# Optimization experiments

Hardware: AMD Instinct MI355X
Metric: run time of the kernel (lower is better)

Reference implementation:

```python
import jax, jax.numpy as jnp
import numpy as np

NUM_HEADS = 8
CHUNK = 64          # dialtion / chunck_size
EPS = 1e-5          # InstanceNorm1d eps
NEG = -1e9


def setup_inputs() -> dict:
    key = jax.random.key(0)
    ks = jax.random.split(key, 8)
    N, C, T = 4, 512, 4096
    x = jax.random.normal(ks[0], (N, C, T), dtype=jnp.float32)
    q = jax.random.normal(ks[1], (N, C, T), dtype=jnp.float32)
    k = jax.random.normal(ks[2], (N, C, T), dtype=jnp.float32)
    v = jax.random.normal(ks[3], (N, C, T), dtype=jnp.float32)
    masks = jnp.ones((N, 1, T), dtype=jnp.float32)
    s = 1.0 / np.sqrt(C)
    W_in = jax.random.normal(ks[4], (3 * C, C), dtype=jnp.float32) * s   # packed q/k/v in-proj
    b_in = jnp.zeros((3 * C,), dtype=jnp.float32)
    W_out = jax.random.normal(ks[5], (C, C), dtype=jnp.float32) * s     # out-proj
    b_out = jnp.zeros((C,), dtype=jnp.float32)
    return {"x": x, "q": q, "k": k, "v": v, "masks": masks,
            "W_in": W_in, "b_in": b_in, "W_out": W_out, "b_out": b_out}


def _chunk_attn(q, k, v, masks, W_in, b_in, W_out, b_out):
    # q,k,v: [N, C, T]; masks: [N, 1, T]
    N, C, T = q.shape
    H, Dh = NUM_HEADS, C // NUM_HEADS
    nc = T // CHUNK
    Wq, Wk, Wv = jnp.split(W_in, 3, axis=0)
    bq, bk, bv = jnp.split(b_in, 3, axis=0)

    def proj(t, W, b):
        # [N,C,T] -> chunked heads [N, nc, CHUNK, H, Dh]
        t = t.transpose(0, 2, 1) @ W.T + b            # [N, T, C]
        return t.reshape(N, nc, CHUNK, H, Dh)

    qh = proj(q, Wq, bq)
    kh = proj(k, Wk, bk)
    vh = proj(v, Wv, bv)

    scale = 1.0 / jnp.sqrt(jnp.asarray(Dh, q.dtype))
    # intra-chunk scores: [N, nc, H, CHUNK, CHUNK]
    scores = jnp.einsum('bnqhd,bnkhd->bnhqk', qh, kh) * scale
    km = masks[:, 0, :].reshape(N, nc, CHUNK)         # key validity per chunk
    scores = scores + jnp.where(km[:, :, None, None, :] > 0, 0.0, NEG)
    attn = jax.nn.softmax(scores, axis=-1)
    out = jnp.einsum('bnhqk,bnkhd->bnqhd', attn, vh).reshape(N, T, C)
    out = out @ W_out.T + b_out                        # [N, T, C]
    out = out.transpose(0, 2, 1) * masks               # [N, C, T], re-mask
    return out


def reference(x, q, k, v, masks, W_in, b_in, W_out, b_out):
    out = _chunk_attn(q, k, v, masks, W_in, b_in, W_out, b_out) + x
    # InstanceNorm1d (affine=False): normalize each (n, c) row over T
    mu = jnp.mean(out, axis=2, keepdims=True)
    var = jnp.mean(jnp.square(out - mu), axis=2, keepdims=True)
    return (out - mu) * jax.lax.rsqrt(var + EPS)
```

## Files before the change

### kernel.cpp

```cpp
#include <hip/hip_runtime.h>
#include <hip/hip_bf16.h>

#define NB 4
#define CC 512
#define TT 4096
#define C3 1536
#define CQK 1024
#define NTC (NB*TT*CC)

typedef __attribute__((ext_vector_type(4))) float f32x4;
typedef __attribute__((ext_vector_type(8))) short short8;
typedef unsigned short ushort;
typedef __attribute__((ext_vector_type(8))) ushort u16x8;

__device__ __forceinline__ ushort f2bf(float f){
    union { float f; unsigned u; } x; x.f = f;
    unsigned r = x.u + 0x7fffu + ((x.u >> 16) & 1u);
    return (ushort)(r >> 16);
}

__device__ __forceinline__ ushort2 pk2bf(float a, float b){
    float2 f2; f2.x = a; f2.y = b;
    __hip_bfloat162 h = __float22bfloat162_rn(f2);
    union { __hip_bfloat162 h2; ushort2 u2; } u; u.h2 = h;
    return u.u2;
}

__device__ __forceinline__ void gload16(const void* g, void* l){
    __builtin_amdgcn_global_load_lds((const __attribute__((address_space(1))) void*)g,
                                     (__attribute__((address_space(3))) void*)l,
                                     16, 0, 0);
}

__device__ __forceinline__ int apos(int m, int cb){
    return (m*8 + ((cb + m + (m >> 3)) & 7))*8;
}

__global__ __launch_bounds__(256) void wcvt(const float* __restrict__ Wi,
                                            const float* __restrict__ Wo,
                                            ushort* __restrict__ Wb,
                                            ushort* __restrict__ Wob){
    int idx0 = blockIdx.x * 1024 + threadIdx.x;
    for (int i = 0; i < 4; ++i){
        int idx = idx0 + i*256;
        const float* src; ushort* dst; int j;
        if (idx < 196608){ src = Wi; dst = Wb;  j = idx; }
        else             { src = Wo; dst = Wob; j = idx - 196608; }
        f32x4 vv = *((const f32x4*)src + j);
        ushort4 o;
        *(ushort2*)&o.x = pk2bf(vv[0], vv[1]);
        *(ushort2*)&o.z = pk2bf(vv[2], vv[3]);
        *((ushort4*)dst + j) = o;
    }
}

__global__ __launch_bounds__(256) void proj_gemm(const float* __restrict__ q,
                                                 const float* __restrict__ k,
                                                 const float* __restrict__ v,
                                                 const ushort* __restrict__ Wb,
                                                 const float* __restrict__ b_in,
                                                 ushort* __restrict__ P,
                                                 ushort* __restrict__ Vt){
    __shared__ __align__(16) ushort smem[40960];
    ushort* sA   = smem;
    ushort* sB0  = smem + 8192;
    ushort* sB1  = smem + 16384;
    float*  Araw = (float*)(smem + 24576);
    const int tid = threadIdx.x;
    const int bid = blockIdx.x;
    const int mtile  = ((bid & 7) << 4) | ((bid >> 3) & 15);
    const int cotile = bid >> 7;
    const int co0 = cotile * 128;
    const int m0  = mtile * 128;
    const int which = co0 >> 9;
    const float* src = (which == 0) ? q : (which == 1) ? k : v;
    const int n  = m0 >> 12, t0 = m0 & 4095;
    const ushort* Bbase = Wb + (size_t)co0*CC;
    const int w = tid >> 6, lane = tid & 63;
    const int wr = w >> 1, wc = w & 1;
    const int l15 = lane & 15, quad = lane >> 4;

    const int rowoff = lane >> 5;
    const int toff   = (lane & 31) * 4;
    const float* Ag = src + (size_t)n*CC*TT + (size_t)(2*w + rowoff)*TT + t0 + toff;
    float* lAr = Araw + (size_t)(2*w)*128;

    const ushort* gB[4]; int lBoff[4];
    for (int i = 0; i < 4; ++i){
        int slot = i*256 + tid;
        int mr = slot >> 3, k8 = slot & 7, kk = k8 ^ (mr & 7);
        gB[i] = Bbase + (size_t)mr*CC + kk*8;
        lBoff[i] = (i*256 + (tid & ~63)) * 8;
    }

    const int cbA = (w << 1) | (lane >> 5);
    const int tA  = lane & 31;

    for (int r = 0; r < 8; ++r)
        gload16(Ag + (size_t)(r*8)*TT, lAr + r*1024);
    for (int i = 0; i < 4; ++i)
        gload16(gB[i], sB0 + lBoff[i]);

    f32x4 acc[4][4] = {};
    for (int kb = 0; kb < 8; ++kb){
        ushort* sBc = (kb & 1) ? sB1 : sB0;
        ushort* sBn = (kb & 1) ? sB0 : sB1;
        __syncthreads();
        f32x4 cur[8];
        #pragma unroll
        for (int j = 0; j < 8; ++j)
            cur[j] = *(const f32x4*)(Araw + (size_t)(cbA*8 + j)*128 + tA*4);
        #pragma unroll
        for (int tj = 0; tj < 4; ++tj){
            int m = tA*4 + tj;
            u16x8 o;
            #pragma unroll
            for (int j = 0; j < 8; j += 2){
                ushort2 p = pk2bf(cur[j][tj], cur[j+1][tj]);
                o[j] = p.x; o[j+1] = p.y;
            }
            *(u16x8*)&sA[apos(m, cbA)] = o;
        }
        __syncthreads();
        if (kb < 7){
            const float* Agn = Ag + (size_t)((kb+1)*64)*TT;
            for (int r = 0; r < 8; ++r)
                gload16(Agn + (size_t)(r*8)*TT, lAr + r*1024);
            for (int i = 0; i < 4; ++i)
                gload16(gB[i] + (kb+1)*64, sBn + lBoff[i]);
        }
        for (int ks = 0; ks < 2; ++ks){
            short8 aF[4], bF[4];
            for (int mi = 0; mi < 4; ++mi){
                int m = wr*64 + mi*16 + l15;
                aF[mi] = *(const short8*)&sA[apos(m, ks*4 + quad)];
            }
            for (int ni = 0; ni < 4; ++ni){
                int m = wc*64 + ni*16 + l15;
                bF[ni] = *(const short8*)&sBc[(m*8 + ((ks*4 + quad) ^ (m & 7)))*8];
            }
            for (int mi = 0; mi < 4; ++mi)
                for (int ni = 0; ni < 4; ++ni)
                    acc[mi][ni] = __builtin_amdgcn_mfma_f32_16x16x32_bf16(
                        aF[mi], bF[ni], acc[mi][ni], 0, 0, 0);
        }
    }

    float bj[4];
    for (int ni = 0; ni < 4; ++ni) bj[ni] = b_in[co0 + wc*64 + ni*16 + l15];

    __syncthreads();
    ushort* sOut = smem;
    if (which < 2){
        for (int mi = 0; mi < 4; ++mi){
            int mrow = wr*64 + mi*16 + quad*4;
            for (int ni = 0; ni < 4; ++ni){
                int col = wc*64 + ni*16 + l15;
                for (int r = 0; r < 4; ++r)
                    sOut[(mrow + r)*136 + col] = f2bf(acc[mi][ni][r] + bj[ni]);
            }
        }
    } else {
        for (int mi = 0; mi < 4; ++mi){
            int mrow = wr*64 + mi*16 + quad*4;
            for (int ni = 0; ni < 4; ++ni){
                int col = wc*64 + ni*16 + l15;
                ushort4 o4;
                o4.x = f2bf(acc[mi][ni][0] + bj[ni]);
                o4.y = f2bf(acc[mi][ni][1] + bj[ni]);
                o4.z = f2bf(acc[mi][ni][2] + bj[ni]);
                o4.w = f2bf(acc[mi][ni][3] + bj[ni]);
                *(ushort4*)&sOut[col*136 + mrow] = o4;
            }
        }
    }
    __syncthreads();
    if (which < 2){
        for (int i = 0; i < 8; ++i){
            int flat = i*256 + tid;
            int row = flat >> 4, cs = (flat & 15)*8;
            u16x8 val = *(const u16x8*)&sOut[row*136 + cs];
            *(u16x8*)(P + (size_t)(m0 + row)*CQK + which*512 + (co0 & 511) + cs) = val;
        }
    } else {
        for (int i = 0; i < 8; ++i){
            int flat = i*256 + tid;
            int row = flat >> 4, cs = (flat & 15)*8;
            int cl = (co0 - 1024) + row;
            int h = cl >> 6, d = cl & 63;
            u16x8 val = *(const u16x8*)&sOut[row*136 + cs];
            *(u16x8*)(Vt + (((size_t)n*8 + h)*64 + d)*TT + t0 + cs) = val;
        }
    }
}

__global__ __launch_bounds__(256) void attn_kernel(const ushort* __restrict__ P,
                                                   const ushort* __restrict__ Vt,
                                                   const float* __restrict__ masks,
                                                   ushort* __restrict__ ctx){
    __shared__ __align__(16) ushort sQ[64*64], sK[64*64], sV[64*64];
    __shared__ __align__(16) ushort sP[64][72];
    __shared__ __align__(16) ushort sO[64*72];
    int bid = blockIdx.x;
    int h = bid & 7, ch = (bid >> 3) & 63, n = bid >> 9;
    const int tid = threadIdx.x, lane = tid & 63, w = tid >> 6;
    const int l15 = lane & 15, quad = lane >> 4;
    const size_t rowbase = (size_t)n*TT + (size_t)ch*64;
    for (int i = 0; i < 2; ++i){
        int slot = i*256 + tid;
        int r = slot >> 3, k8 = slot & 7, kk = k8 ^ (r & 7);
        int lbase = (i*256 + (tid & ~63)) * 8;
        const ushort* gq = P + (rowbase + r)*CQK + h*64 + kk*8;
        gload16(gq,        sQ + lbase);
        gload16(gq + 512,  sK + lbase);
        const ushort* gv = Vt + (((size_t)n*8 + h)*64 + r)*TT + ch*64 + kk*8;
        gload16(gv,        sV + lbase);
    }
    __syncthreads();
    const int m0w = w*16;
    short8 aQ[2]; f32x4 accS[4] = {};
    for (int ks = 0; ks < 2; ++ks){
        int m = m0w + l15;
        aQ[ks] = *(const short8*)&sQ[(m*8 + ((ks*4 + quad) ^ (m & 7)))*8];
    }
    for (int ni = 0; ni < 4; ++ni)
        for (int ks = 0; ks < 2; ++ks){
            int m = ni*16 + l15;
            short8 bK = *(const short8*)&sK[(m*8 + ((ks*4 + quad) ^ (m & 7)))*8];
            accS[ni] = __builtin_amdgcn_mfma_f32_16x16x32_bf16(aQ[ks], bK, accS[ni], 0,0,0);
        }
    float madd[4];
    for (int ni = 0; ni < 4; ++ni){
        float mv = masks[(size_t)n*TT + ch*64 + ni*16 + l15];
        madd[ni] = (mv > 0.f) ? 0.f : -1e9f;
    }
    float s[4][4];
    for (int ni = 0; ni < 4; ++ni)
        for (int r = 0; r < 4; ++r) s[ni][r] = accS[ni][r]*0.125f + madd[ni];
    float ex[4][4];
    for (int r = 0; r < 4; ++r){
        float m1 = fmaxf(fmaxf(s[0][r], s[1][r]), fmaxf(s[2][r], s[3][r]));
        for (int d = 1; d < 16; d <<= 1) m1 = fmaxf(m1, __shfl_xor(m1, d));
        float a = 0.f;
        for (int ni = 0; ni < 4; ++ni){ float e = __expf(s[ni][r] - m1); ex[ni][r] = e; a += e; }
        for (int d = 1; d < 16; d <<= 1) a += __shfl_xor(a, d);
        float rs = 1.0f / a;
        for (int ni = 0; ni < 4; ++ni)
            sP[m0w + quad*4 + r][ni*16 + l15] = f2bf(ex[ni][r] * rs);
    }
    short8 aP[2]; f32x4 accO[4] = {};
    for (int ks = 0; ks < 2; ++ks)
        aP[ks] = *(const short8*)&sP[m0w + l15][ks*32 + quad*8];
    for (int ni = 0; ni < 4; ++ni)
        for (int ks = 0; ks < 2; ++ks){
            int m = ni*16 + l15;
            short8 bV = *(const short8*)&sV[(m*8 + ((ks*4 + quad) ^ (m & 7)))*8];
            accO[ni] = __builtin_amdgcn_mfma_f32_16x16x32_bf16(aP[ks], bV, accO[ni], 0,0,0);
        }
    for (int ni = 0; ni < 4; ++ni)
        for (int r = 0; r < 4; ++r)
            sO[(m0w + quad*4 + r)*72 + ni*16 + l15] = f2bf(accO[ni][r]);
    __syncthreads();
    for (int i = 0; i < 2; ++i){
        int flat = i*256 + tid;
        int row = flat >> 3, cs = (flat & 7)*8;
        u16x8 val = *(const u16x8*)&sO[row*72 + cs];
        *(u16x8*)(ctx + (rowbase + row)*CC + h*64 + cs) = val;
    }
}

__global__ __launch_bounds__(256) void out_gemm(const ushort* __restrict__ ctx,
                                                const ushort* __restrict__ Wob,
                                                const float* __restrict__ b_out,
                                                const float* __restrict__ x,
                                                const float* __restrict__ masks,
                                                float* __restrict__ out){
    __shared__ __align__(16) ushort smem[16896];
    ushort* sA = smem;
    ushort* sB = smem + 128*64;
    float* fOut = (float*)smem;
    const int tid = threadIdx.x;
    const int bid = blockIdx.x;
    const int mtile  = ((bid & 7) << 4) | ((bid >> 3) & 15);
    const int cotile = bid >> 7;
    const int co0 = cotile * 64;
    const int m0  = mtile * 128;
    const int n = m0 >> 12, t0 = m0 & 4095;
    const ushort* Abase = ctx + (size_t)m0*CC;
    const ushort* Bbase = Wob + (size_t)co0*CC;
    const int w = tid >> 6, lane = tid & 63;
    const int wr = w >> 1, wc = w & 1;
    const int l15 = lane & 15, quad = lane >> 4;

    const ushort* gA[4]; ushort* lA[4];
    const ushort* gB[2]; ushort* lB[2];
    for (int i = 0; i < 4; ++i){
        int slot = i*256 + tid;
        int m = slot >> 3, k8 = slot & 7, kk = k8 ^ (m & 7);
        gA[i] = Abase + (size_t)m*CC + kk*8;
        lA[i] = sA + (i*256 + (tid & ~63)) * 8;
    }
    for (int i = 0; i < 2; ++i){
        int slot = i*256 + tid;
        int m = slot >> 3, k8 = slot & 7, kk = k8 ^ (m & 7);
        gB[i] = Bbase + (size_t)m*CC + kk*8;
        lB[i] = sB + (i*256 + (tid & ~63)) * 8;
    }

    f32x4 acc[4][2] = {};
    for (int kb = 0; kb < 8; ++kb){
        __syncthreads();
        for (int i = 0; i < 4; ++i) gload16(gA[i] + kb*64, lA[i]);
        for (int i = 0; i < 2; ++i) gload16(gB[i] + kb*64, lB[i]);
        __syncthreads();
        for (int ks = 0; ks < 2; ++ks){
            short8 aF[4], bF[2];
            for (int mi = 0; mi < 4; ++mi){
                int m = wr*64 + mi*16 + l15;
                aF[mi] = *(const short8*)&sA[(m*8 + ((ks*4 + quad) ^ (m & 7)))*8];
            }
            for (int ni = 0; ni < 2; ++ni){
                int m = wc*32 + ni*16 + l15;
                bF[ni] = *(const short8*)&sB[(m*8 + ((ks*4 + quad) ^ (m & 7)))*8];
            }
            for (int mi = 0; mi < 4; ++mi)
                for (int ni = 0; ni < 2; ++ni)
                    acc[mi][ni] = __builtin_amdgcn_mfma_f32_16x16x32_bf16(
                        aF[mi], bF[ni], acc[mi][ni], 0, 0, 0);
        }
    }
    float bo[2];
    for (int ni = 0; ni < 2; ++ni) bo[ni] = b_out[co0 + wc*32 + ni*16 + l15];

    __syncthreads();
    for (int mi = 0; mi < 4; ++mi){
        int tl = wr*64 + mi*16 + quad*4;
        for (int ni = 0; ni < 2; ++ni){
            int cl = wc*32 + ni*16 + l15;
            f32x4 vv;
            for (int r = 0; r < 4; ++r) vv[r] = acc[mi][ni][r] + bo[ni];
            *(f32x4*)&fOut[cl*132 + tl] = vv;
        }
    }
    __syncthreads();
    for (int i = 0; i < 8; ++i){
        int flat = i*256 + tid;
        int co = flat >> 5, ts = (flat & 31)*4;
        f32x4 a = *(const f32x4*)&fOut[co*132 + ts];
        f32x4 mk = *(const f32x4*)(masks + (size_t)n*TT + t0 + ts);
        f32x4 xv = *(const f32x4*)(x + ((size_t)n*CC + co0 + co)*TT + t0 + ts);
        f32x4 o;
        for (int r = 0; r < 4; ++r) o[r] = a[r]*mk[r] + xv[r];
        *(f32x4*)(out + ((size_t)n*CC + co0 + co)*TT + t0 + ts) = o;
    }
}

__global__ __launch_bounds__(256) void inorm(float* __restrict__ out){
    __shared__ float sS[4], sQ2[4];
    float* row = out + (size_t)blockIdx.x * TT;
    f32x4 vbuf[4];
    float s = 0.f, ss = 0.f;
    for (int i = 0; i < 4; ++i){
        f32x4 vv = *(const f32x4*)(row + (size_t)(i*256 + threadIdx.x)*4);
        vbuf[i] = vv;
        for (int r = 0; r < 4; ++r){ s += vv[r]; ss += vv[r]*vv[r]; }
    }
    for (int d = 1; d < 64; d <<= 1){ s += __shfl_xor(s, d); ss += __shfl_xor(ss, d); }
    int w = threadIdx.x >> 6;
    if ((threadIdx.x & 63) == 0){ sS[w] = s; sQ2[w] = ss; }
    __syncthreads();
    s  = sS[0] + sS[1] + sS[2] + sS[3];
    ss = sQ2[0] + sQ2[1] + sQ2[2] + sQ2[3];
    float mean = s * (1.0f/TT);
    float var  = ss * (1.0f/TT) - mean*mean;
    float rstd = rsqrtf(var + 1e-5f);
    for (int i = 0; i < 4; ++i){
        f32x4 vv = vbuf[i], o;
        for (int r = 0; r < 4; ++r) o[r] = (vv[r] - mean) * rstd;
        *(f32x4*)(row + (size_t)(i*256 + threadIdx.x)*4) = o;
    }
}

extern "C" void kernel_launch(void* const* d_in, const int* in_sizes, int n_in,
                              void* d_out, int out_size, void* d_ws, size_t ws_size,
                              hipStream_t stream) {
    const float* x     = (const float*)d_in[0];
    const float* q     = (const float*)d_in[1];
    const float* k     = (const float*)d_in[2];
    const float* v     = (const float*)d_in[3];
    const float* masks = (const float*)d_in[4];
    const float* W_in  = (const float*)d_in[5];
    const float* b_in  = (const float*)d_in[6];
    const float* W_out = (const float*)d_in[7];
    const float* b_out = (const float*)d_in[8];
    float* out = (float*)d_out;

    ushort* ws  = (ushort*)d_ws;
    ushort* ctx = ws;
    ushort* Wb  = ws + (size_t)NTC;
    ushort* Wob = Wb + 786432;
    ushort* P   = Wob + 262144;
    ushort* Vt  = P + (size_t)NB*TT*CQK;

    wcvt<<<256, 256, 0, stream>>>(W_in, W_out, Wb, Wob);
    proj_gemm<<<1536, 256, 0, stream>>>(q, k, v, Wb, b_in, P, Vt);
    attn_kernel<<<2048, 256, 0, stream>>>(P, Vt, masks, ctx);
    out_gemm<<<1024, 256, 0, stream>>>(ctx, Wob, b_out, x, masks, out);
    inorm<<<2048, 256, 0, stream>>>(out);
}
```

Before: 238.9 us.

## Register-stage fp32 A tiles in proj GEMM and double-buffer out GEMM

```diff
diff --git a/kernel.cpp b/kernel.cpp
--- a/kernel.cpp
+++ b/kernel.cpp
@@ -54,18 +54,17 @@
     }
 }
 
-__global__ __launch_bounds__(256) void proj_gemm(const float* __restrict__ q,
-                                                 const float* __restrict__ k,
-                                                 const float* __restrict__ v,
-                                                 const ushort* __restrict__ Wb,
-                                                 const float* __restrict__ b_in,
-                                                 ushort* __restrict__ P,
-                                                 ushort* __restrict__ Vt){
-    __shared__ __align__(16) ushort smem[40960];
-    ushort* sA   = smem;
-    ushort* sB0  = smem + 8192;
-    ushort* sB1  = smem + 16384;
-    float*  Araw = (float*)(smem + 24576);
+__global__ __launch_bounds__(256, 3) void proj_gemm(const float* __restrict__ q,
+                                                    const float* __restrict__ k,
+                                                    const float* __restrict__ v,
+                                                    const ushort* __restrict__ Wb,
+                                                    const float* __restrict__ b_in,
+                                                    ushort* __restrict__ P,
+                                                    ushort* __restrict__ Vt){
+    __shared__ __align__(16) ushort smem[24576];
+    ushort* sA  = smem;
+    ushort* sB0 = smem + 8192;
+    ushort* sB1 = smem + 16384;
     const int tid = threadIdx.x;
     const int bid = blockIdx.x;
     const int mtile  = ((bid & 7) << 4) | ((bid >> 3) & 15);
@@ -79,71 +78,82 @@
     const int w = tid >> 6, lane = tid & 63;
     const int wr = w >> 1, wc = w & 1;
     const int l15 = lane & 15, quad = lane >> 4;
-
-    const int rowoff = lane >> 5;
-    const int toff   = (lane & 31) * 4;
-    const float* Ag = src + (size_t)n*CC*TT + (size_t)(2*w + rowoff)*TT + t0 + toff;
-    float* lAr = Araw + (size_t)(2*w)*128;
-
-    const ushort* gB[4]; int lBoff[4];
-    for (int i = 0; i < 4; ++i){
-        int slot = i*256 + tid;
-        int mr = slot >> 3, k8 = slot & 7, kk = k8 ^ (mr & 7);
-        gB[i] = Bbase + (size_t)mr*CC + kk*8;
-        lBoff[i] = (i*256 + (tid & ~63)) * 8;
-    }
-
-    const int cbA = (w << 1) | (lane >> 5);
-    const int tA  = lane & 31;
-
-    for (int r = 0; r < 8; ++r)
-        gload16(Ag + (size_t)(r*8)*TT, lAr + r*1024);
+    const int hlf = lane >> 5, tq = lane & 31;
+
+    const int mrB = tid >> 3;
+    const int kkB = (tid & 7) ^ (mrB & 7);
+    const ushort* gB0 = Bbase + (size_t)mrB*CC + kkB*8;
+    const int lB0 = (tid & ~63) * 8;
+
+    const float* Ab = src + (size_t)n*CC*TT + t0 + tq*4;
+    const int ce0 = w*16 + hlf*2;
+
+    f32x4 a0[4], a1[4];
+    #pragma unroll
+    for (int u = 0; u < 4; ++u){
+        a0[u] = *(const f32x4*)(Ab + (size_t)(ce0 + u*4    )*TT);
+        a1[u] = *(const f32x4*)(Ab + (size_t)(ce0 + u*4 + 1)*TT);
+    }
+    #pragma unroll
     for (int i = 0; i < 4; ++i)
-        gload16(gB[i], sB0 + lBoff[i]);
+        gload16(gB0 + (size_t)i*32*CC, sB0 + lB0 + i*2048);
+    #pragma unroll
+    for (int u = 0; u < 4; ++u){
+        int ce = ce0 + u*4;
+        int cb = ce >> 3, off = ce & 7;
+        #pragma unroll
+        for (int j = 0; j < 4; ++j)
+            *(ushort2*)&sA[apos(tq*4 + j, cb) + off] = pk2bf(a0[u][j], a1[u][j]);
+    }
+    __syncthreads();
 
     f32x4 acc[4][4] = {};
     for (int kb = 0; kb < 8; ++kb){
         ushort* sBc = (kb & 1) ? sB1 : sB0;
         ushort* sBn = (kb & 1) ? sB0 : sB1;
-        __syncthreads();
-        f32x4 cur[8];
+        if (kb < 7){
+            const float* Abn = Ab + (size_t)((kb+1)*64)*TT;
+            #pragma unroll
+            for (int u = 0; u < 4; ++u){
+                a0[u] = *(const f32x4*)(Abn + (size_t)(ce0 + u*4    )*TT);
+                a1[u] = *(const f32x4*)(Abn + (size_t)(ce0 + u*4 + 1)*TT);
+            }
+            #pragma unroll
+            for (int i = 0; i < 4; ++i)
+                gload16(gB0 + (size_t)i*32*CC + (kb+1)*64, sBn + lB0 + i*2048);
+        }
         #pragma unroll
-        for (int j = 0; j < 8; ++j)
-            cur[j] = *(const f32x4*)(Araw + (size_t)(cbA*8 + j)*128 + tA*4);
-        #pragma unroll
-        for (int tj = 0; tj < 4; ++tj){
-            int m = tA*4 + tj;
-            u16x8 o;
-            #pragma unroll
-            for (int j = 0; j < 8; j += 2){
-                ushort2 p = pk2bf(cur[j][tj], cur[j+1][tj]);
-                o[j] = p.x; o[j+1] = p.y;
-            }
-            *(u16x8*)&sA[apos(m, cbA)] = o;
-        }
-        __syncthreads();
-        if (kb < 7){
-            const float* Agn = Ag + (size_t)((kb+1)*64)*TT;
-            for (int r = 0; r < 8; ++r)
-                gload16(Agn + (size_t)(r*8)*TT, lAr + r*1024);
-            for (int i = 0; i < 4; ++i)
-                gload16(gB[i] + (kb+1)*64, sBn + lBoff[i]);
-        }
         for (int ks = 0; ks < 2; ++ks){
             short8 aF[4], bF[4];
+            #pragma unroll
             for (int mi = 0; mi < 4; ++mi){
                 int m = wr*64 + mi*16 + l15;
                 aF[mi] = *(const short8*)&sA[apos(m, ks*4 + quad)];
             }
+            #pragma unroll
             for (int ni = 0; ni < 4; ++ni){
                 int m = wc*64 + ni*16 + l15;
                 bF[ni] = *(const short8*)&sBc[(m*8 + ((ks*4 + quad) ^ (m & 7)))*8];
             }
+            #pragma unroll
             for (int mi = 0; mi < 4; ++mi)
+                #pragma unroll
                 for (int ni = 0; ni < 4; ++ni)
                     acc[mi][ni] = __builtin_amdgcn_mfma_f32_16x16x32_bf16(
                         aF[mi], bF[ni], acc[mi][ni], 0, 0, 0);
         }
+        __syncthreads();
+        if (kb < 7){
+            #pragma unroll
+            for (int u = 0; u < 4; ++u){
+                int ce = ce0 + u*4;
+                int cb = ce >> 3, off = ce & 7;
+                #pragma unroll
+                for (int j = 0; j < 4; ++j)
+                    *(ushort2*)&sA[apos(tq*4 + j, cb) + off] = pk2bf(a0[u][j], a1[u][j]);
+            }
+        }
+        __syncthreads();
     }
 
     float bj[4];
@@ -275,9 +285,11 @@
                                                 const float* __restrict__ x,
                                                 const float* __restrict__ masks,
                                                 float* __restrict__ out){
-    __shared__ __align__(16) ushort smem[16896];
-    ushort* sA = smem;
-    ushort* sB = smem + 128*64;
+    __shared__ __align__(16) ushort smem[24576];
+    ushort* sA0 = smem;
+    ushort* sA1 = smem + 8192;
+    ushort* sB0 = smem + 16384;
+    ushort* sB1 = smem + 20480;
     float* fOut = (float*)smem;
     const int tid = threadIdx.x;
     const int bid = blockIdx.x;
@@ -292,38 +304,48 @@
     const int wr = w >> 1, wc = w & 1;
     const int l15 = lane & 15, quad = lane >> 4;
 
-    const ushort* gA[4]; ushort* lA[4];
-    const ushort* gB[2]; ushort* lB[2];
-    for (int i = 0; i < 4; ++i){
-        int slot = i*256 + tid;
-        int m = slot >> 3, k8 = slot & 7, kk = k8 ^ (m & 7);
-        gA[i] = Abase + (size_t)m*CC + kk*8;
-        lA[i] = sA + (i*256 + (tid & ~63)) * 8;
-    }
-    for (int i = 0; i < 2; ++i){
-        int slot = i*256 + tid;
-        int m = slot >> 3, k8 = slot & 7, kk = k8 ^ (m & 7);
-        gB[i] = Bbase + (size_t)m*CC + kk*8;
-        lB[i] = sB + (i*256 + (tid & ~63)) * 8;
-    }
+    const int mr = tid >> 3;
+    const int kk = (tid & 7) ^ (mr & 7);
+    const ushort* gA0 = Abase + (size_t)mr*CC + kk*8;
+    const ushort* gB0 = Bbase + (size_t)mr*CC + kk*8;
+    const int lS = (tid & ~63) * 8;
+
+    #pragma unroll
+    for (int i = 0; i < 4; ++i) gload16(gA0 + (size_t)i*32*CC, sA0 + lS + i*2048);
+    #pragma unroll
+    for (int i = 0; i < 2; ++i) gload16(gB0 + (size_t)i*32*CC, sB0 + lS + i*2048);
 
     f32x4 acc[4][2] = {};
     for (int kb = 0; kb < 8; ++kb){
+        ushort* sAc = (kb & 1) ? sA1 : sA0;
+        ushort* sBc = (kb & 1) ? sB1 : sB0;
+        ushort* sAn = (kb & 1) ? sA0 : sA1;
+        ushort* sBn = (kb & 1) ? sB0 : sB1;
         __syncthreads();
-        for (int i = 0; i < 4; ++i) gload16(gA[i] + kb*64, lA[i]);
-        for (int i = 0; i < 2; ++i) gload16(gB[i] + kb*64, lB[i]);
-        __syncthreads();
+        if (kb < 7){
+            #pragma unroll
+            for (int i = 0; i < 4; ++i)
+                gload16(gA0 + (size_t)i*32*CC + (kb+1)*64, sAn + lS + i*2048);
+            #pragma unroll
+            for (int i = 0; i < 2; ++i)
+                gload16(gB0 + (size_t)i*32*CC + (kb+1)*64, sBn + lS + i*2048);
+        }
+        #pragma unroll
         for (int ks = 0; ks < 2; ++ks){
             short8 aF[4], bF[2];
+            #pragma unroll
             for (int mi = 0; mi < 4; ++mi){
                 int m = wr*64 + mi*16 + l15;
-                aF[mi] = *(const short8*)&sA[(m*8 + ((ks*4 + quad) ^ (m & 7)))*8];
-            }
+                aF[mi] = *(const short8*)&sAc[(m*8 + ((ks*4 + quad) ^ (m & 7)))*8];
+            }
+            #pragma unroll
             for (int ni = 0; ni < 2; ++ni){
                 int m = wc*32 + ni*16 + l15;
-                bF[ni] = *(const short8*)&sB[(m*8 + ((ks*4 + quad) ^ (m & 7)))*8];
-            }
+                bF[ni] = *(const short8*)&sBc[(m*8 + ((ks*4 + quad) ^ (m & 7)))*8];
+            }
+            #pragma unroll
             for (int mi = 0; mi < 4; ++mi)
+                #pragma unroll
                 for (int ni = 0; ni < 2; ++ni)
                     acc[mi][ni] = __builtin_amdgcn_mfma_f32_16x16x32_bf16(
                         aF[mi], bF[ni], acc[mi][ni], 0, 0, 0);
```

Result: no change. 243.0 us (+1.7%).

## Load GEMM operands directly from global into MFMA fragments, drop LDS staging

Applied to the files above, without the earlier changes.

```diff
diff --git a/kernel.cpp b/kernel.cpp
--- a/kernel.cpp
+++ b/kernel.cpp
@@ -30,10 +30,6 @@
     __builtin_amdgcn_global_load_lds((const __attribute__((address_space(1))) void*)g,
                                      (__attribute__((address_space(3))) void*)l,
                                      16, 0, 0);
-}
-
-__device__ __forceinline__ int apos(int m, int cb){
-    return (m*8 + ((cb + m + (m >> 3)) & 7))*8;
 }
 
 __global__ __launch_bounds__(256) void wcvt(const float* __restrict__ Wi,
@@ -61,11 +57,7 @@
                                                  const float* __restrict__ b_in,
                                                  ushort* __restrict__ P,
                                                  ushort* __restrict__ Vt){
-    __shared__ __align__(16) ushort smem[40960];
-    ushort* sA   = smem;
-    ushort* sB0  = smem + 8192;
-    ushort* sB1  = smem + 16384;
-    float*  Araw = (float*)(smem + 24576);
+    __shared__ __align__(16) ushort sOut[128*136];
     const int tid = threadIdx.x;
     const int bid = blockIdx.x;
     const int mtile  = ((bid & 7) << 4) | ((bid >> 3) & 15);
@@ -75,102 +67,76 @@
     const int which = co0 >> 9;
     const float* src = (which == 0) ? q : (which == 1) ? k : v;
     const int n  = m0 >> 12, t0 = m0 & 4095;
-    const ushort* Bbase = Wb + (size_t)co0*CC;
     const int w = tid >> 6, lane = tid & 63;
     const int wr = w >> 1, wc = w & 1;
     const int l15 = lane & 15, quad = lane >> 4;
 
-    const int rowoff = lane >> 5;
-    const int toff   = (lane & 31) * 4;
-    const float* Ag = src + (size_t)n*CC*TT + (size_t)(2*w + rowoff)*TT + t0 + toff;
-    float* lAr = Araw + (size_t)(2*w)*128;
-
-    const ushort* gB[4]; int lBoff[4];
-    for (int i = 0; i < 4; ++i){
-        int slot = i*256 + tid;
-        int mr = slot >> 3, k8 = slot & 7, kk = k8 ^ (mr & 7);
-        gB[i] = Bbase + (size_t)mr*CC + kk*8;
-        lBoff[i] = (i*256 + (tid & ~63)) * 8;
-    }
-
-    const int cbA = (w << 1) | (lane >> 5);
-    const int tA  = lane & 31;
-
-    for (int r = 0; r < 8; ++r)
-        gload16(Ag + (size_t)(r*8)*TT, lAr + r*1024);
-    for (int i = 0; i < 4; ++i)
-        gload16(gB[i], sB0 + lBoff[i]);
+    const float* Abase = src + (size_t)n*CC*TT + (size_t)(quad*8)*TT
+                             + t0 + wc*64 + l15;
+    const ushort* Wfb = Wb + (size_t)(co0 + wr*64 + l15)*CC + quad*8;
 
     f32x4 acc[4][4] = {};
+    #pragma unroll
     for (int kb = 0; kb < 8; ++kb){
-        ushort* sBc = (kb & 1) ? sB1 : sB0;
-        ushort* sBn = (kb & 1) ? sB0 : sB1;
-        __syncthreads();
-        f32x4 cur[8];
         #pragma unroll
-        for (int j = 0; j < 8; ++j)
-            cur[j] = *(const f32x4*)(Araw + (size_t)(cbA*8 + j)*128 + tA*4);
-        #pragma unroll
-        for (int tj = 0; tj < 4; ++tj){
-            int m = tA*4 + tj;
-            u16x8 o;
-            #pragma unroll
-            for (int j = 0; j < 8; j += 2){
-                ushort2 p = pk2bf(cur[j][tj], cur[j+1][tj]);
-                o[j] = p.x; o[j+1] = p.y;
+        for (int ks = 0; ks < 2; ++ks){
+            const int c0 = kb*64 + ks*32;
+            short8 aW[4];
+            #pragma unroll
+            for (int mi = 0; mi < 4; ++mi)
+                aW[mi] = *(const short8*)(Wfb + (size_t)(mi*16)*CC + c0);
+            short8 bA[4];
+            #pragma unroll
+            for (int ni = 0; ni < 4; ++ni){
+                const float* p = Abase + (size_t)c0*TT + ni*16;
+                float v0,v1,v2,v3,v4,v5,v6,v7;
+                v0 = p[0*(size_t)TT]; v1 = p[1*(size_t)TT];
+                v2 = p[2*(size_t)TT]; v3 = p[3*(size_t)TT];
+                v4 = p[4*(size_t)TT]; v5 = p[5*(size_t)TT];
+                v6 = p[6*(size_t)TT]; v7 = p[7*(size_t)TT];
+                ushort2 p0 = pk2bf(v0, v1), p1 = pk2bf(v2, v3);
+                ushort2 p2 = pk2bf(v4, v5), p3 = pk2bf(v6, v7);
+                short8 o;
+                o[0]=(short)p0.x; o[1]=(short)p0.y;
+                o[2]=(short)p1.x; o[3]=(short)p1.y;
+                o[4]=(short)p2.x; o[5]=(short)p2.y;
+                o[6]=(short)p3.x; o[7]=(short)p3.y;
+                bA[ni] = o;
             }
-            *(u16x8*)&sA[apos(m, cbA)] = o;
-        }
-        __syncthreads();
-        if (kb < 7){
-            const float* Agn = Ag + (size_t)((kb+1)*64)*TT;
-            for (int r = 0; r < 8; ++r)
-                gload16(Agn + (size_t)(r*8)*TT, lAr + r*1024);
-            for (int i = 0; i < 4; ++i)
-                gload16(gB[i] + (kb+1)*64, sBn + lBoff[i]);
-        }
-        for (int ks = 0; ks < 2; ++ks){
-            short8 aF[4], bF[4];
-            for (int mi = 0; mi < 4; ++mi){
-                int m = wr*64 + mi*16 + l15;
-                aF[mi] = *(const short8*)&sA[apos(m, ks*4 + quad)];
-            }
-            for (int ni = 0; ni < 4; ++ni){
-                int m = wc*64 + ni*16 + l15;
-                bF[ni] = *(const short8*)&sBc[(m*8 + ((ks*4 + quad) ^ (m & 7)))*8];
-            }
+            #pragma unroll
             for (int mi = 0; mi < 4; ++mi)
+                #pragma unroll
                 for (int ni = 0; ni < 4; ++ni)
                     acc[mi][ni] = __builtin_amdgcn_mfma_f32_16x16x32_bf16(
-                        aF[mi], bF[ni], acc[mi][ni], 0, 0, 0);
-        }
-    }
-
-    float bj[4];
-    for (int ni = 0; ni < 4; ++ni) bj[ni] = b_in[co0 + wc*64 + ni*16 + l15];
-
-    __syncthreads();
-    ushort* sOut = smem;
+                        aW[mi], bA[ni], acc[mi][ni], 0, 0, 0);
+        }
+    }
+
+    f32x4 bj[4];
+    #pragma unroll
+    for (int mi = 0; mi < 4; ++mi)
+        bj[mi] = *(const f32x4*)(b_in + co0 + wr*64 + mi*16 + quad*4);
+
     if (which < 2){
         for (int mi = 0; mi < 4; ++mi){
-            int mrow = wr*64 + mi*16 + quad*4;
+            int cl = wr*64 + mi*16 + quad*4;
             for (int ni = 0; ni < 4; ++ni){
-                int col = wc*64 + ni*16 + l15;
-                for (int r = 0; r < 4; ++r)
-                    sOut[(mrow + r)*136 + col] = f2bf(acc[mi][ni][r] + bj[ni]);
+                int tl = wc*64 + ni*16 + l15;
+                ushort4 o4;
+                o4.x = f2bf(acc[mi][ni][0] + bj[mi][0]);
+                o4.y = f2bf(acc[mi][ni][1] + bj[mi][1]);
+                o4.z = f2bf(acc[mi][ni][2] + bj[mi][2]);
+                o4.w = f2bf(acc[mi][ni][3] + bj[mi][3]);
+                *(ushort4*)&sOut[tl*136 + cl] = o4;
             }
         }
     } else {
         for (int mi = 0; mi < 4; ++mi){
-            int mrow = wr*64 + mi*16 + quad*4;
+            int cl = wr*64 + mi*16 + quad*4;
             for (int ni = 0; ni < 4; ++ni){
-                int col = wc*64 + ni*16 + l15;
-                ushort4 o4;
-                o4.x = f2bf(acc[mi][ni][0] + bj[ni]);
-                o4.y = f2bf(acc[mi][ni][1] + bj[ni]);
-                o4.z = f2bf(acc[mi][ni][2] + bj[ni]);
-                o4.w = f2bf(acc[mi][ni][3] + bj[ni]);
-                *(ushort4*)&sOut[col*136 + mrow] = o4;
+                int tl = wc*64 + ni*16 + l15;
+                for (int r = 0; r < 4; ++r)
+                    sOut[(cl + r)*136 + tl] = f2bf(acc[mi][ni][r] + bj[mi][r]);
             }
         }
     }
@@ -202,7 +168,8 @@
     __shared__ __align__(16) ushort sP[64][72];
     __shared__ __align__(16) ushort sO[64*72];
     int bid = blockIdx.x;
-    int h = bid & 7, ch = (bid >> 3) & 63, n = bid >> 9;
+    int l = (bid & 7)*256 + (bid >> 3);
+    int h = l & 7, ch = (l >> 3) & 63, n = l >> 9;
     const int tid = threadIdx.x, lane = tid & 63, w = tid >> 6;
     const int l15 = lane & 15, quad = lane >> 4;
     const size_t rowbase = (size_t)n*TT + (size_t)ch*64;
@@ -275,55 +242,38 @@
                                                 const float* __restrict__ x,
                                                 const float* __restrict__ masks,
                                                 float* __restrict__ out){
-    __shared__ __align__(16) ushort smem[16896];
-    ushort* sA = smem;
-    ushort* sB = smem + 128*64;
-    float* fOut = (float*)smem;
+    __shared__ __align__(16) float fOut[64*132];
     const int tid = threadIdx.x;
     const int bid = blockIdx.x;
-    const int mtile  = ((bid & 7) << 4) | ((bid >> 3) & 15);
-    const int cotile = bid >> 7;
+    const int l = (bid & 7)*128 + (bid >> 3);
+    const int cotile = l & 7;
+    const int mtile  = l >> 3;
     const int co0 = cotile * 64;
     const int m0  = mtile * 128;
     const int n = m0 >> 12, t0 = m0 & 4095;
-    const ushort* Abase = ctx + (size_t)m0*CC;
-    const ushort* Bbase = Wob + (size_t)co0*CC;
     const int w = tid >> 6, lane = tid & 63;
     const int wr = w >> 1, wc = w & 1;
     const int l15 = lane & 15, quad = lane >> 4;
 
-    const ushort* gA[4]; ushort* lA[4];
-    const ushort* gB[2]; ushort* lB[2];
-    for (int i = 0; i < 4; ++i){
-        int slot = i*256 + tid;
-        int m = slot >> 3, k8 = slot & 7, kk = k8 ^ (m & 7);
-        gA[i] = Abase + (size_t)m*CC + kk*8;
-        lA[i] = sA + (i*256 + (tid & ~63)) * 8;
-    }
-    for (int i = 0; i < 2; ++i){
-        int slot = i*256 + tid;
-        int m = slot >> 3, k8 = slot & 7, kk = k8 ^ (m & 7);
-        gB[i] = Bbase + (size_t)m*CC + kk*8;
-        lB[i] = sB + (i*256 + (tid & ~63)) * 8;
-    }
+    const ushort* Afb = ctx + (size_t)(m0 + wr*64 + l15)*CC + quad*8;
+    const ushort* Wfb = Wob + (size_t)(co0 + wc*32 + l15)*CC + quad*8;
 
     f32x4 acc[4][2] = {};
+    #pragma unroll
     for (int kb = 0; kb < 8; ++kb){
-        __syncthreads();
-        for (int i = 0; i < 4; ++i) gload16(gA[i] + kb*64, lA[i]);
-        for (int i = 0; i < 2; ++i) gload16(gB[i] + kb*64, lB[i]);
-        __syncthreads();
+        #pragma unroll
         for (int ks = 0; ks < 2; ++ks){
+            const int c0 = kb*64 + ks*32;
             short8 aF[4], bF[2];
-            for (int mi = 0; mi < 4; ++mi){
-                int m = wr*64 + mi*16 + l15;
-                aF[mi] = *(const short8*)&sA[(m*8 + ((ks*4 + quad) ^ (m & 7)))*8];
-            }
-            for (int ni = 0; ni < 2; ++ni){
-                int m = wc*32 + ni*16 + l15;
-                bF[ni] = *(const short8*)&sB[(m*8 + ((ks*4 + quad) ^ (m & 7)))*8];
-            }
+            #pragma unroll
             for (int mi = 0; mi < 4; ++mi)
+                aF[mi] = *(const short8*)(Afb + (size_t)(mi*16)*CC + c0);
+            #pragma unroll
+            for (int ni = 0; ni < 2; ++ni)
+                bF[ni] = *(const short8*)(Wfb + (size_t)(ni*16)*CC + c0);
+            #pragma unroll
+            for (int mi = 0; mi < 4; ++mi)
+                #pragma unroll
                 for (int ni = 0; ni < 2; ++ni)
                     acc[mi][ni] = __builtin_amdgcn_mfma_f32_16x16x32_bf16(
                         aF[mi], bF[ni], acc[mi][ni], 0, 0, 0);
@@ -332,7 +282,6 @@
     float bo[2];
     for (int ni = 0; ni < 2; ++ni) bo[ni] = b_out[co0 + wc*32 + ni*16 + l15];
 
-    __syncthreads();
     for (int mi = 0; mi < 4; ++mi){
         int tl = wr*64 + mi*16 + quad*4;
         for (int ni = 0; ni < 2; ++ni){
```

Measured after the change: 309.2 us. 1.29x slower.
